# Kernel tuning notes

Hardware: AMD Instinct MI355X
Metric: run time of the kernel (lower is better)

The kernel has to match this reference:

```python
import jax, jax.numpy as jnp
import numpy as np

B, T = 128, 100
DZ, DA, DU, K, DOBS, H = 64, 32, 8, 8, 16, 128
JITTER = 1e-4  # _safe_cholesky: sym + jitter*I, then first try adds 1.0*jitter*I again


def setup_inputs() -> dict:
    key = jax.random.key(0)
    ks = jax.random.split(key, 10)
    eye_z = jnp.eye(DZ, dtype=jnp.float32)
    # stable-ish per-component transition matrices
    A_mats = 0.9 * eye_z[None] + 0.05 * jax.random.normal(ks[0], (K, DZ, DZ), jnp.float32)
    B_mats = 0.1 * jax.random.normal(ks[1], (K, DZ, DU), jnp.float32)
    C_mats = 0.3 * jax.random.normal(ks[2], (K, DA, DZ), jnp.float32)
    a_seq = jax.random.normal(ks[3], (B, T, DA), jnp.float32)
    h_obs = jax.random.normal(ks[4], (B, DOBS), jnp.float32)
    u_seq = jax.random.normal(ks[5], (B, T, DU), jnp.float32)
    mask = jnp.ones((B, T), jnp.float32)
    a_0 = jnp.zeros((1, DA), jnp.float32)          # nn.Parameter a_0
    P_0 = 10.0 * eye_z                              # 10 * eye(dim_z)
    Q = 0.05 * eye_z                                # Q_std * eye(dim_z)
    R = 0.05 * jnp.eye(DA, dtype=jnp.float32)       # R_std * eye(dim_a)
    din = DA + DOBS + DU
    s = 1.0 / float(np.sqrt(H))
    W_ih = s * jax.random.normal(ks[6], (3 * H, din), jnp.float32)
    W_hh = s * jax.random.normal(ks[7], (3 * H, H), jnp.float32)
    b_ih = jnp.zeros((3 * H,), jnp.float32)
    b_hh = jnp.zeros((3 * H,), jnp.float32)
    W_out = s * jax.random.normal(ks[8], (K, H), jnp.float32)
    b_out = jnp.zeros((K,), jnp.float32)
    return dict(a_seq=a_seq, h_obs=h_obs, u_seq=u_seq, mask=mask,
                A_mats=A_mats, B_mats=B_mats, C_mats=C_mats,
                a_0=a_0, P_0=P_0, Q=Q, R=R,
                W_ih=W_ih, W_hh=W_hh, b_ih=b_ih, b_hh=b_hh,
                W_out=W_out, b_out=b_out, epoch=100)


def _sym(M):
    return 0.5 * (M + jnp.swapaxes(M, -1, -2))


def _gru_alpha(x, h, W_ih, W_hh, b_ih, b_hh, W_out, b_out):
    # GRU-cell alpha_net: mixture weights over K components
    gi = x @ W_ih.T + b_ih
    gh = h @ W_hh.T + b_hh
    ir, iz, inn = jnp.split(gi, 3, axis=-1)
    hr, hz, hn = jnp.split(gh, 3, axis=-1)
    r = jax.nn.sigmoid(ir + hr)
    zg = jax.nn.sigmoid(iz + hz)
    n = jnp.tanh(inn + r * hn)
    h_new = (1.0 - zg) * n + zg * h
    alpha = jax.nn.softmax(h_new @ W_out.T + b_out, axis=-1)
    return alpha, h_new


def _kalman_forward(a_seq, h_obs, u_seq, mask, A_mats, B_mats, C_mats,
                    a_0, P_0, Q, R, W_ih, W_hh, b_ih, b_hh, W_out, b_out):
    Bsz = a_seq.shape[0]
    I = jnp.eye(DZ, dtype=a_seq.dtype)

    def mix(alpha):
        A = jnp.einsum('bk,kij->bij', alpha, A_mats)
        Bc = jnp.einsum('bk,kij->bij', alpha, B_mats)
        C = jnp.einsum('bk,kij->bij', alpha, C_mats)
        return A, Bc, C

    def alpha_net(a, u, h):
        x = jnp.concatenate([a, h_obs, u], axis=-1)
        return _gru_alpha(x, h, W_ih, W_hh, b_ih, b_hh, W_out, b_out)

    gru_h = jnp.zeros((Bsz, H), a_seq.dtype)
    a_prev = jnp.broadcast_to(a_0, (Bsz, DA))
    alpha0, gru_h = alpha_net(a_prev, u_seq[:, 0], gru_h)
    A_k0, B_k0, C_k0 = mix(alpha0)

    z0 = jnp.zeros((Bsz, DZ), a_seq.dtype)
    P0 = jnp.broadcast_to(P_0, (Bsz, DZ, DZ))

    def step(carry, inp):
        z_prev, P, h, A_k, B_k, C_k = carry
        a_k, u_k, m_k = inp  # [B,da], [B,du], [B]
        mk = m_k[:, None]
        # predict with matrices chosen at previous step
        z = jnp.einsum('bij,bj->bi', A_k, z_prev) + jnp.einsum('bij,bj->bi', B_k, u_k)
        a_hat = jnp.einsum('bij,bj->bi', C_k, z)
        r_k = a_k - a_hat
        CP = jnp.einsum('bij,bjk->bik', C_k, P)                      # C P
        S = jnp.einsum('bik,bjk->bij', CP, C_k) + R                   # C P C^T + R
        # K = solve(S^T, C P^T)^T  (i.e. K = P C^T S^{-1})
        CPt = jnp.einsum('bij,bkj->bik', C_k, P)
        Kg = jnp.swapaxes(jnp.linalg.solve(jnp.swapaxes(S, -1, -2), CPt), -1, -2)
        Kg = Kg * m_k[:, None, None]
        IKC = I - jnp.einsum('bij,bjk->bik', Kg, C_k)
        # Joseph form update
        P_filt = (jnp.einsum('bij,bjk,blk->bil', IKC, P, IKC)
                  + jnp.einsum('bij,jk,blk->bil', Kg, R, Kg))
        P_filt = _sym(P_filt)
        z_mean = z + jnp.einsum('bij,bj->bi', Kg, r_k)
        L = jnp.linalg.cholesky(_sym(P_filt) + 2.0 * JITTER * I)      # safe cholesky
        z_filt = z_mean                                               # dist.mean
        a_filt = jnp.einsum('bij,bj->bi', C_k, z_filt)
        a_k_hat = mk * a_k + (1.0 - mk) * a_filt
        C_old = C_k
        alpha, h = alpha_net(a_k_hat, u_k, h)
        A_n, B_n, C_n = mix(alpha)
        z_pred = (jnp.einsum('bij,bj->bi', A_n, z_filt)
                  + jnp.einsum('bij,bj->bi', B_n, u_k))
        a_pred = jnp.einsum('bij,bj->bi', C_n, z_pred)
        P_pred = _sym(jnp.einsum('bij,bjk,blk->bil', A_n, P_filt, A_n) + Q)
        carry = (z_filt, P_pred, h, A_n, B_n, C_n)
        out = (z_filt, P_filt, z_pred, P_pred, alpha, a_filt, a_pred,
               S, z_mean, L, A_n, B_n, C_old)
        return carry, out

    xs = (jnp.swapaxes(a_seq, 0, 1), jnp.swapaxes(u_seq, 0, 1), jnp.swapaxes(mask, 0, 1))
    _, outs = jax.lax.scan(step, (z0, P0, gru_h, A_k0, B_k0, C_k0), xs)
    # scan outputs are [T, B, ...] -> [B, T, ...]
    (z_filt, P_filt, z_pred, P_pred, alpha_seq, a_filt, a_pred,
     S_pred, z_means, z_scale_tril, A_seq, B_seq, C_seq) = jax.tree.map(
        lambda x: jnp.swapaxes(x, 0, 1), outs)
    return (z_filt, P_filt, z_pred, a_filt, a_pred, P_pred, alpha_seq,
            A_seq, B_seq, C_seq, z_means, z_scale_tril, S_pred)


def reference(a_seq, h_obs, u_seq, mask, A_mats, B_mats, C_mats,
              a_0, P_0, Q, R, W_ih, W_hh, b_ih, b_hh, W_out, b_out, epoch):
    # epoch >= warmup/burn-in thresholds (all 0), so no detach branches apply
    return _kalman_forward(a_seq, h_obs, u_seq, mask, A_mats, B_mats, C_mats,
                           a_0, P_0, Q, R, W_ih, W_hh, b_ih, b_hh, W_out, b_out)
```

## Files before the change

### kernel.cpp

```cpp
#include <hip/hip_runtime.h>

typedef float f4 __attribute__((ext_vector_type(4)));

#define NT 256
#define BB 128
#define BT 100
#define DZc 64
#define DAc 32
#define DUc 8
#define KMIX 8
#define DOBSc 16
#define HG 128
#define DINc 56

#define O_ZFILT   0LL
#define O_PFILT   819200LL
#define O_ZPRED   53248000LL
#define O_AFILT   54067200LL
#define O_APRED   54476800LL
#define O_PPRED   54886400LL
#define O_ALPHA   107315200LL
#define O_ASEQ    107417600LL
#define O_BSEQ    159846400LL
#define O_CSEQ    166400000LL
#define O_ZMEAN   192614400LL
#define O_LTRIL   193433600LL
#define O_SPRED   245862400LL

__device__ __forceinline__ float dot4(f4 a, f4 b) {
    return a[0]*b[0] + a[1]*b[1] + a[2]*b[2] + a[3]*b[3];
}

struct SMem {
    float P[DZc][68];
    float A[DZc][68];
    float AT[DZc][65];
    float Wk[DZc][68];
    float Qm[DZc][68];
    float C[DAc][68];
    float CP[DAc][68];
    float Xm[DAc][68];
    float S[DAc][33];
    float Rm[DAc][33];
    float dinv[DAc];
    float col[64];
    float Bm[DZc][8];
    float z[DZc], zp[DZc], zn[DZc];
    float h[HG], hn[HG];
    float gh[3*HG], gi[3*HG];
    float x[64];
    float ak[DAc], rvec[DAc];
    float akN[DAc];
    float ubuf[2][8];
    float mkN;
    float lg[8];
    float mk;
};

template<bool EMIT>
__device__ __forceinline__ void mix_apply(SMem& s, int tid, size_t bt, const float* al8,
    const float* __restrict__ A_mats, const float* __restrict__ B_mats,
    const float* __restrict__ C_mats, float* __restrict__ out)
{
    const f4* A4 = (const f4*)A_mats;
    const f4* B4 = (const f4*)B_mats;
    const f4* C4 = (const f4*)C_mats;
    #pragma unroll 2
    for (int e = 0; e < 4; ++e) {
        int i4 = tid + e*256;
        f4 acc = {0.f,0.f,0.f,0.f};
        #pragma unroll
        for (int k = 0; k < 8; ++k) acc += al8[k] * A4[k*1024 + i4];
        int row = i4 >> 4, cb = (i4 & 15) * 4;
        *(f4*)&s.A[row][cb] = acc;
        s.AT[cb][row] = acc[0]; s.AT[cb+1][row] = acc[1];
        s.AT[cb+2][row] = acc[2]; s.AT[cb+3][row] = acc[3];
        if (EMIT) *(f4*)&out[O_ASEQ + bt*4096 + (size_t)i4*4] = acc;
    }
    if (tid < 128) {
        int i4 = tid;
        f4 acc = {0.f,0.f,0.f,0.f};
        #pragma unroll
        for (int k = 0; k < 8; ++k) acc += al8[k] * B4[k*128 + i4];
        *(f4*)&s.Bm[i4>>1][(i4&1)*4] = acc;
        if (EMIT) *(f4*)&out[O_BSEQ + bt*512 + (size_t)i4*4] = acc;
    }
    #pragma unroll 1
    for (int e = 0; e < 2; ++e) {
        int i4 = tid + e*256;
        f4 acc = {0.f,0.f,0.f,0.f};
        #pragma unroll
        for (int k = 0; k < 8; ++k) acc += al8[k] * C4[k*512 + i4];
        *(f4*)&s.C[i4>>4][(i4&15)*4] = acc;
    }
}

__global__ void __launch_bounds__(NT, 1)
kalman_seq(const float* __restrict__ a_seq, const float* __restrict__ h_obs,
           const float* __restrict__ u_seq, const float* __restrict__ mask,
           const float* __restrict__ A_mats, const float* __restrict__ B_mats,
           const float* __restrict__ C_mats, const float* __restrict__ a_0,
           const float* __restrict__ P_0, const float* __restrict__ Q,
           const float* __restrict__ R, const float* __restrict__ W_ih,
           const float* __restrict__ W_hh, const float* __restrict__ b_ih,
           const float* __restrict__ b_hh, const float* __restrict__ W_out,
           const float* __restrict__ b_out, float* __restrict__ out)
{
    __shared__ SMem s;
    const int b = blockIdx.x;
    const int tid = threadIdx.x;
    const int r4 = (tid >> 4) << 2;
    const int c4 = (tid & 15) << 2;

    for (int idx = tid; idx < DZc*DZc; idx += NT) {
        s.P[idx >> 6][idx & 63]  = P_0[idx];
        s.Qm[idx >> 6][idx & 63] = Q[idx];
    }
    for (int idx = tid; idx < DAc*DAc; idx += NT) s.Rm[idx >> 5][idx & 31] = R[idx];
    if (tid < HG) s.h[tid] = 0.f;
    if (tid < DZc) { s.z[tid] = 0.f; s.zp[tid] = 0.f; }
    if (tid < DAc)                 s.x[tid] = a_0[tid];
    else if (tid < DAc + DOBSc)    s.x[tid] = h_obs[b*DOBSc + (tid - DAc)];
    else if (tid < DINc)           s.x[tid] = u_seq[(size_t)b*BT*DUc + (tid - DAc - DOBSc)];
    if (tid >= 128 && tid < 160)      s.akN[tid-128] = a_seq[(size_t)b*BT*DAc + (tid-128)];
    else if (tid >= 160 && tid < 168) { s.ubuf[0][tid-160] = u_seq[(size_t)b*BT*DUc + (tid-160)];
                                        s.ubuf[1][tid-160] = 0.f; }
    else if (tid == 168)              s.mkN = mask[(size_t)b*BT];
    __syncthreads();

    for (int g = tid; g < 3*HG; g += NT) {
        const float* wi = W_ih + (size_t)g * DINc;
        f4 ai = {0.f,0.f,0.f,0.f};
        #pragma unroll 7
        for (int q = 0; q < 14; ++q) ai += *(const f4*)(wi + q*4) * *(const f4*)&s.x[q*4];
        s.gi[g] = ai[0]+ai[1]+ai[2]+ai[3] + b_ih[g];
        s.gh[g] = b_hh[g];
    }
    __syncthreads();
    if (tid < HG) {
        float r  = 1.f / (1.f + expf(-(s.gi[tid] + s.gh[tid])));
        float zg = 1.f / (1.f + expf(-(s.gi[HG+tid] + s.gh[HG+tid])));
        float n  = tanhf(s.gi[2*HG+tid] + r * s.gh[2*HG+tid]);
        s.h[tid] = (1.f - zg) * n;
    }
    __syncthreads();
    if (tid < KMIX) {
        const float* wo = W_out + tid * HG;
        f4 acc = {0.f,0.f,0.f,0.f};
        #pragma unroll 8
        for (int q = 0; q < 32; ++q) acc += *(const f4*)(wo + q*4) * *(const f4*)&s.h[q*4];
        s.lg[tid] = acc[0]+acc[1]+acc[2]+acc[3] + b_out[tid];
    }
    __syncthreads();
    {
        float lg[8];
        #pragma unroll
        for (int k = 0; k < 8; ++k) lg[k] = s.lg[k];
        float mx = lg[0];
        #pragma unroll
        for (int k = 1; k < 8; ++k) mx = fmaxf(mx, lg[k]);
        float al[8]; float sum = 0.f;
        #pragma unroll
        for (int k = 0; k < 8; ++k) { al[k] = expf(lg[k] - mx); sum += al[k]; }
        float rs = 1.f / sum;
        #pragma unroll
        for (int k = 0; k < 8; ++k) al[k] *= rs;
        mix_apply<false>(s, tid, 0, al, A_mats, B_mats, C_mats, out);
    }
    __syncthreads();

    for (int t = 0; t < BT; ++t) {
        const size_t bt = (size_t)b * BT + t;
        const int cur = t & 1;

        if (tid < 64) {
            float acc = s.zp[tid];
            #pragma unroll
            for (int q = 0; q < DUc; ++q)
                acc += s.Bm[tid][q] * (s.ubuf[cur][q] - s.ubuf[cur^1][q]);
            s.zp[tid] = acc;
        } else if (tid < 96) {
            float av = s.akN[tid-64];
            s.ak[tid-64] = av;
            s.x[tid-64] = av;
        } else if (tid < 104) {
            s.x[48 + (tid-96)] = s.ubuf[cur][tid-96];
        } else if (tid == 104) {
            s.mk = s.mkN;
        }
        __syncthreads();
        const float mkv = s.mk;
        const bool mk1 = (mkv == 1.0f);

        {
            const int r = tid >> 3;
            const int c8 = (tid & 7) * 8;
            f4 acc0 = {0.f,0.f,0.f,0.f}, acc1 = {0.f,0.f,0.f,0.f};
            #pragma unroll 4
            for (int k4 = 0; k4 < 16; ++k4) {
                f4 cr = *(const f4*)&s.C[r][k4*4];
                #pragma unroll
                for (int kk = 0; kk < 4; ++kk) {
                    float cv = cr[kk];
                    acc0 += cv * *(const f4*)&s.P[k4*4+kk][c8];
                    acc1 += cv * *(const f4*)&s.P[k4*4+kk][c8+4];
                }
            }
            *(f4*)&s.CP[r][c8]   = acc0;
            *(f4*)&s.CP[r][c8+4] = acc1;
        }
        if (tid < DAc) {
            float acc = 0.f;
            #pragma unroll 4
            for (int k4 = 0; k4 < 16; ++k4)
                acc += dot4(*(const f4*)&s.C[tid][k4*4], *(const f4*)&s.zp[k4*4]);
            s.rvec[tid] = s.ak[tid] - acc;
        }
        __syncthreads();

        {
            const int r = tid >> 3;
            const int cb = (tid & 7) * 4;
            f4 acc = {0.f,0.f,0.f,0.f};
            #pragma unroll 4
            for (int k4 = 0; k4 < 16; ++k4) {
                f4 a = *(const f4*)&s.CP[r][k4*4];
                #pragma unroll
                for (int j = 0; j < 4; ++j)
                    acc[j] += dot4(a, *(const f4*)&s.C[cb+j][k4*4]);
            }
            f4 rm = {s.Rm[r][cb], s.Rm[r][cb+1], s.Rm[r][cb+2], s.Rm[r][cb+3]};
            f4 v = acc + rm;
            s.S[r][cb] = v[0]; s.S[r][cb+1] = v[1]; s.S[r][cb+2] = v[2]; s.S[r][cb+3] = v[3];
            *(f4*)&out[O_SPRED + bt*1024 + (size_t)r*32 + cb] = v;
        }
        __syncthreads();

        if (tid < 64) {
            const int lane = tid;
            const int l = lane & 31;
            float row[32];
            #pragma unroll
            for (int j = 0; j < 32; ++j) row[j] = s.S[l][j];
            #pragma unroll
            for (int k = 0; k < 32; ++k) {
                if (lane < 32) s.col[lane] = row[k];
                __threadfence_block();
                float cb[32];
                #pragma unroll
                for (int jv = 0; jv < 8; ++jv) {
                    if (jv*4 + 3 >= k) {
                        f4 cv = *(const f4*)&s.col[jv*4];
                        cb[jv*4] = cv[0]; cb[jv*4+1] = cv[1];
                        cb[jv*4+2] = cv[2]; cb[jv*4+3] = cv[3];
                    }
                }
                float dv = 1.0f / cb[k];
                if (lane == k) s.dinv[k] = dv;
                float fm = (l > k) ? (row[k] * dv) : 0.f;
                #pragma unroll
                for (int j = k+1; j < 32; ++j)
                    row[j] -= fm * cb[j];
                __threadfence_block();
            }
            if (lane < 32) {
                #pragma unroll
                for (int j = 0; j < 32; ++j) s.S[l][j] = row[j];
            }
            __threadfence_block();
            float v[32];
            #pragma unroll
            for (int r = 0; r < 32; ++r) v[r] = s.CP[r][lane];
            #pragma unroll
            for (int r = 0; r < 32; ++r) {
                float acc = v[r];
                #pragma unroll
                for (int k = 0; k < r; ++k) acc -= s.S[r][k] * v[k];
                v[r] = s.dinv[r] * acc;
            }
            #pragma unroll
            for (int r = 30; r >= 0; --r) {
                float acc = 0.f;
                #pragma unroll
                for (int k = r+1; k < 32; ++k) acc += s.S[k][r] * v[k];
                v[r] -= s.dinv[r] * acc;
            }
            float accz = 0.f;
            #pragma unroll
            for (int r = 0; r < 32; ++r) {
                s.Xm[r][lane] = v[r];
                accz += v[r] * s.rvec[r];
            }
            s.zn[lane] = s.zp[lane] + mkv * accz;
            __threadfence_block();
            if (lane < DAc) {
                float acc = 0.f;
                #pragma unroll 4
                for (int k4 = 0; k4 < 16; ++k4)
                    acc += dot4(*(const f4*)&s.C[lane][k4*4], *(const f4*)&s.zn[k4*4]);
                out[O_AFILT + bt*DAc + lane] = acc;
                if (!mk1) s.x[lane] = mkv * s.ak[lane] + (1.f - mkv) * acc;
            }
        } else if (tid < 192) {
            const int idx = tid - 64;
            const float* wir = W_ih + (size_t)idx * DINc;
            const float* wiz = W_ih + (size_t)(HG + idx) * DINc;
            const float* win = W_ih + (size_t)(2*HG + idx) * DINc;
            const float* whr = W_hh + (size_t)idx * HG;
            const float* whz = W_hh + (size_t)(HG + idx) * HG;
            const float* whn = W_hh + (size_t)(2*HG + idx) * HG;
            f4 air = {0.f,0.f,0.f,0.f}, aiz = {0.f,0.f,0.f,0.f}, ain = {0.f,0.f,0.f,0.f};
            #pragma unroll 4
            for (int q = 0; q < 14; ++q) {
                f4 xv = *(const f4*)&s.x[q*4];
                air += *(const f4*)(wir + q*4) * xv;
                aiz += *(const f4*)(wiz + q*4) * xv;
                ain += *(const f4*)(win + q*4) * xv;
            }
            f4 ahr = {0.f,0.f,0.f,0.f}, ahz = {0.f,0.f,0.f,0.f}, ahn = {0.f,0.f,0.f,0.f};
            #pragma unroll 4
            for (int q = 0; q < 32; ++q) {
                f4 hv = *(const f4*)&s.h[q*4];
                ahr += *(const f4*)(whr + q*4) * hv;
                ahz += *(const f4*)(whz + q*4) * hv;
                ahn += *(const f4*)(whn + q*4) * hv;
            }
            float gir = air[0]+air[1]+air[2]+air[3] + b_ih[idx];
            float giz = aiz[0]+aiz[1]+aiz[2]+aiz[3] + b_ih[HG + idx];
            float gin = ain[0]+ain[1]+ain[2]+ain[3] + b_ih[2*HG + idx];
            float ghr = ahr[0]+ahr[1]+ahr[2]+ahr[3] + b_hh[idx];
            float ghz = ahz[0]+ahz[1]+ahz[2]+ahz[3] + b_hh[HG + idx];
            float ghn = ahn[0]+ahn[1]+ahn[2]+ahn[3] + b_hh[2*HG + idx];
            float r  = 1.f / (1.f + expf(-(gir + ghr)));
            float zg = 1.f / (1.f + expf(-(giz + ghz)));
            float n  = tanhf(gin + r * ghn);
            s.hn[idx] = (1.f - zg) * n + zg * s.h[idx];
        } else {
            const int l = tid - 192;
            #pragma unroll 2
            for (int e = 0; e < 8; ++e) {
                int i4 = l + e*64;
                *(f4*)&out[O_CSEQ + bt*2048 + (size_t)i4*4] = *(const f4*)&s.C[i4>>4][(i4&15)*4];
            }
        }
        __syncthreads();

        float pfA = 0.f, pfU = 0.f, pfM = 0.f;
        {
            const int t2 = (t+1 < BT) ? (t+1) : t;
            const size_t bt2 = (size_t)b*BT + t2;
            if (tid >= 192 && tid < 224)      pfA = a_seq[bt2*DAc + (tid-192)];
            else if (tid >= 224 && tid < 232) pfU = u_seq[bt2*DUc + (tid-224)];
            else if (tid == 232)              pfM = mask[bt2];
        }

        {
            const float coef = (mkv*mkv - 2.f*mkv) * 0.5f;
            f4 acc0 = {0.f,0.f,0.f,0.f}, acc1 = {0.f,0.f,0.f,0.f};
            f4 acc2 = {0.f,0.f,0.f,0.f}, acc3 = {0.f,0.f,0.f,0.f};
            #pragma unroll 4
            for (int l = 0; l < DAc; ++l) {
                f4 cpc = *(const f4*)&s.CP[l][c4];
                f4 xc  = *(const f4*)&s.Xm[l][c4];
                f4 cpr = *(const f4*)&s.CP[l][r4];
                f4 xr  = *(const f4*)&s.Xm[l][r4];
                acc0 += xr[0]*cpc + cpr[0]*xc;
                acc1 += xr[1]*cpc + cpr[1]*xc;
                acc2 += xr[2]*cpc + cpr[2]*xc;
                acc3 += xr[3]*cpc + cpr[3]*xc;
            }
            #pragma unroll
            for (int i = 0; i < 4; ++i) {
                const int row = r4 + i;
                f4 g = (i==0) ? acc0 : (i==1) ? acc1 : (i==2) ? acc2 : acc3;
                f4 p = *(const f4*)&s.P[row][c4];
                f4 v = p + coef * g;
                *(f4*)&s.P[row][c4] = v;
                *(f4*)&out[O_PFILT + bt*4096 + (size_t)row*64 + c4] = v;
            }
        }
        if (tid < DZc) {
            float v = s.zn[tid];
            out[O_ZFILT + bt*DZc + tid] = v;
            out[O_ZMEAN + bt*DZc + tid] = v;
            s.z[tid] = v;
        }

        if (!mk1) {
            __syncthreads();
            for (int g = tid; g < 3*HG; g += NT) {
                const float* wi = W_ih + (size_t)g * DINc;
                const float* wh = W_hh + (size_t)g * HG;
                f4 ai = {0.f,0.f,0.f,0.f}, ah = {0.f,0.f,0.f,0.f};
                #pragma unroll 7
                for (int q = 0; q < 14; ++q) ai += *(const f4*)(wi + q*4) * *(const f4*)&s.x[q*4];
                #pragma unroll 8
                for (int q = 0; q < 32; ++q) ah += *(const f4*)(wh + q*4) * *(const f4*)&s.h[q*4];
                s.gi[g] = ai[0]+ai[1]+ai[2]+ai[3] + b_ih[g];
                s.gh[g] = ah[0]+ah[1]+ah[2]+ah[3] + b_hh[g];
            }
            __syncthreads();
            if (tid < HG) {
                float gi0 = s.gi[tid], gi1 = s.gi[HG+tid], gi2 = s.gi[2*HG+tid];
                float gh0 = s.gh[tid], gh1 = s.gh[HG+tid], gh2 = s.gh[2*HG+tid];
                float hold = s.h[tid];
                float r  = 1.f / (1.f + expf(-(gi0 + gh0)));
                float zg = 1.f / (1.f + expf(-(gi1 + gh1)));
                float n  = tanhf(gi2 + r * gh2);
                s.hn[tid] = (1.f - zg) * n + zg * hold;
            }
            __syncthreads();
        }

        {
            const int lane = tid & 63;
            const int g = lane >> 3;
            const int cb = (lane & 7) * 16;
            f4 a4 = {0.f,0.f,0.f,0.f};
            #pragma unroll
            for (int q = 0; q < 4; ++q)
                a4 += *(const f4*)(W_out + (size_t)g*HG + cb + q*4) * *(const f4*)&s.hn[cb + q*4];
            float acc = a4[0]+a4[1]+a4[2]+a4[3];
            acc += __shfl_xor(acc, 1); acc += __shfl_xor(acc, 2); acc += __shfl_xor(acc, 4);
            float lg[8];
            #pragma unroll
            for (int k = 0; k < 8; ++k) lg[k] = __shfl(acc, k*8) + b_out[k];
            float mx = lg[0];
            #pragma unroll
            for (int k = 1; k < 8; ++k) mx = fmaxf(mx, lg[k]);
            float al[8]; float sum = 0.f;
            #pragma unroll
            for (int k = 0; k < 8; ++k) { al[k] = expf(lg[k] - mx); sum += al[k]; }
            float rs = 1.f / sum;
            #pragma unroll
            for (int k = 0; k < 8; ++k) al[k] *= rs;
            if (tid < 8) out[O_ALPHA + bt*8 + tid] = al[tid];
            mix_apply<true>(s, tid, bt, al, A_mats, B_mats, C_mats, out);
        }
        if (tid < HG) s.h[tid] = s.hn[tid];
        __syncthreads();

        if (tid < 64) {
            float acc = 0.f;
            #pragma unroll 8
            for (int k = 0; k < DZc; ++k) acc += s.AT[k][tid] * s.z[k];
            #pragma unroll
            for (int q = 0; q < DUc; ++q) acc += s.Bm[tid][q] * s.ubuf[cur][q];
            s.zp[tid] = acc;
            out[O_ZPRED + bt*DZc + tid] = acc;
        }
        {
            f4 acc[4] = {{0.f,0.f,0.f,0.f},{0.f,0.f,0.f,0.f},{0.f,0.f,0.f,0.f},{0.f,0.f,0.f,0.f}};
            #pragma unroll 2
            for (int k4 = 0; k4 < 16; ++k4) {
                f4 ar0 = *(const f4*)&s.A[r4+0][k4*4];
                f4 ar1 = *(const f4*)&s.A[r4+1][k4*4];
                f4 ar2 = *(const f4*)&s.A[r4+2][k4*4];
                f4 ar3 = *(const f4*)&s.A[r4+3][k4*4];
                #pragma unroll
                for (int kk = 0; kk < 4; ++kk) {
                    f4 bv = *(const f4*)&s.P[k4*4+kk][c4];
                    acc[0] += ar0[kk] * bv; acc[1] += ar1[kk] * bv;
                    acc[2] += ar2[kk] * bv; acc[3] += ar3[kk] * bv;
                }
            }
            #pragma unroll
            for (int i = 0; i < 4; ++i)
                *(f4*)&s.Wk[r4+i][c4] = acc[i];
        }
        __syncthreads();

        {
            f4 acc[4] = {{0.f,0.f,0.f,0.f},{0.f,0.f,0.f,0.f},{0.f,0.f,0.f,0.f},{0.f,0.f,0.f,0.f}};
            #pragma unroll 2
            for (int k4 = 0; k4 < 16; ++k4) {
                f4 w0 = *(const f4*)&s.Wk[r4+0][k4*4];
                f4 w1 = *(const f4*)&s.Wk[r4+1][k4*4];
                f4 w2 = *(const f4*)&s.Wk[r4+2][k4*4];
                f4 w3 = *(const f4*)&s.Wk[r4+3][k4*4];
                #pragma unroll
                for (int kk = 0; kk < 4; ++kk) {
                    f4 av = *(const f4*)&s.AT[k4*4+kk][c4];
                    acc[0] += w0[kk] * av; acc[1] += w1[kk] * av;
                    acc[2] += w2[kk] * av; acc[3] += w3[kk] * av;
                }
            }
            #pragma unroll
            for (int i = 0; i < 4; ++i) {
                const int row = r4 + i;
                f4 q = *(const f4*)&s.Qm[row][c4];
                f4 v = acc[i] + q;
                *(f4*)&s.P[row][c4] = v;
                *(f4*)&out[O_PPRED + bt*4096 + (size_t)row*64 + c4] = v;
            }
        }
        if (tid < DAc) {
            float acc = 0.f;
            #pragma unroll 4
            for (int k4 = 0; k4 < 16; ++k4)
                acc += dot4(*(const f4*)&s.C[tid][k4*4], *(const f4*)&s.zp[k4*4]);
            out[O_APRED + bt*DAc + tid] = acc;
        }
        if (tid >= 192 && tid < 224)      s.akN[tid-192] = pfA;
        else if (tid >= 224 && tid < 232) s.ubuf[(t+1)&1][tid-224] = pfU;
        else if (tid == 232)              s.mkN = pfM;
        __syncthreads();
    }
}

__global__ void __launch_bounds__(64)
chol_batch(float* __restrict__ out)
{
    __shared__ float M[DZc][65];
    __shared__ float sd[DZc];
    const size_t bt = blockIdx.x;
    const int lane = threadIdx.x;
    const float* src = out + O_PFILT + bt*4096;
    #pragma unroll 4
    for (int e = 0; e < 16; ++e) {
        int i4 = lane + e*64;
        f4 v = *(const f4*)(src + (size_t)i4*4);
        int row = i4 >> 4, cb = (i4 & 15) * 4;
        M[row][cb] = v[0]; M[row][cb+1] = v[1]; M[row][cb+2] = v[2]; M[row][cb+3] = v[3];
    }
    __syncthreads();
    M[lane][lane] += 2.0e-4f;
    __syncthreads();
    for (int k = 0; k < DZc; ++k) {
        __threadfence_block();
        float mkk = M[k][k];
        if (lane == k) sd[k] = sqrtf(mkk);
        if (lane > k) {
            float f = M[lane][k] / mkk;
            for (int j = k + 1; j <= lane; ++j)
                M[lane][j] -= f * M[j][k];
        }
    }
    __threadfence_block();
    for (int k = 0; k < lane; ++k) M[lane][k] /= sd[k];
    M[lane][lane] = sd[lane];
    for (int k = lane + 1; k < DZc; ++k) M[lane][k] = 0.f;
    __syncthreads();
    float* dst = out + O_LTRIL + bt*4096;
    #pragma unroll 4
    for (int e = 0; e < 16; ++e) {
        int i4 = lane + e*64;
        int row = i4 >> 4, cb = (i4 & 15) * 4;
        f4 v = {M[row][cb], M[row][cb+1], M[row][cb+2], M[row][cb+3]};
        *(f4*)(dst + (size_t)i4*4) = v;
    }
}

extern "C" void kernel_launch(void* const* d_in, const int* in_sizes, int n_in,
                              void* d_out, int out_size, void* d_ws, size_t ws_size,
                              hipStream_t stream) {
    const float* a_seq  = (const float*)d_in[0];
    const float* h_obs  = (const float*)d_in[1];
    const float* u_seq  = (const float*)d_in[2];
    const float* mask   = (const float*)d_in[3];
    const float* A_mats = (const float*)d_in[4];
    const float* B_mats = (const float*)d_in[5];
    const float* C_mats = (const float*)d_in[6];
    const float* a_0    = (const float*)d_in[7];
    const float* P_0    = (const float*)d_in[8];
    const float* Q      = (const float*)d_in[9];
    const float* R      = (const float*)d_in[10];
    const float* W_ih   = (const float*)d_in[11];
    const float* W_hh   = (const float*)d_in[12];
    const float* b_ih   = (const float*)d_in[13];
    const float* b_hh   = (const float*)d_in[14];
    const float* W_out  = (const float*)d_in[15];
    const float* b_out  = (const float*)d_in[16];
    float* out = (float*)d_out;

    kalman_seq<<<dim3(BB), dim3(NT), 0, stream>>>(a_seq, h_obs, u_seq, mask,
        A_mats, B_mats, C_mats, a_0, P_0, Q, R, W_ih, W_hh, b_ih, b_hh, W_out, b_out, out);
    chol_batch<<<dim3(BB*BT), dim3(64), 0, stream>>>(out);
}
```

Measured before the change: 6.335 ms.

## Fold per-step input staging into previous step and double-buffer Cholesky column

New measurement: 6.328 ms. No clear change (-0.1%).

```diff
diff --git a/kernel.cpp b/kernel.cpp
--- a/kernel.cpp
+++ b/kernel.cpp
@@ -43,16 +43,14 @@
     float S[DAc][33];
     float Rm[DAc][33];
     float dinv[DAc];
-    float col[64];
+    float col[2][64];
     float Bm[DZc][8];
     float z[DZc], zp[DZc], zn[DZc];
     float h[HG], hn[HG];
     float gh[3*HG], gi[3*HG];
     float x[64];
     float ak[DAc], rvec[DAc];
-    float akN[DAc];
     float ubuf[2][8];
-    float mkN;
     float lg[8];
     float mk;
 };
@@ -118,14 +116,11 @@
     }
     for (int idx = tid; idx < DAc*DAc; idx += NT) s.Rm[idx >> 5][idx & 31] = R[idx];
     if (tid < HG) s.h[tid] = 0.f;
-    if (tid < DZc) { s.z[tid] = 0.f; s.zp[tid] = 0.f; }
+    if (tid < DZc) s.z[tid] = 0.f;
     if (tid < DAc)                 s.x[tid] = a_0[tid];
     else if (tid < DAc + DOBSc)    s.x[tid] = h_obs[b*DOBSc + (tid - DAc)];
     else if (tid < DINc)           s.x[tid] = u_seq[(size_t)b*BT*DUc + (tid - DAc - DOBSc)];
-    if (tid >= 128 && tid < 160)      s.akN[tid-128] = a_seq[(size_t)b*BT*DAc + (tid-128)];
-    else if (tid >= 160 && tid < 168) { s.ubuf[0][tid-160] = u_seq[(size_t)b*BT*DUc + (tid-160)];
-                                        s.ubuf[1][tid-160] = 0.f; }
-    else if (tid == 168)              s.mkN = mask[(size_t)b*BT];
+    if (tid >= 160 && tid < 168)   s.ubuf[0][tid-160] = u_seq[(size_t)b*BT*DUc + (tid-160)];
     __syncthreads();
 
     for (int g = tid; g < 3*HG; g += NT) {
@@ -169,26 +164,23 @@
     }
     __syncthreads();
 
+    if (tid < 64) {
+        float acc = 0.f;
+        #pragma unroll
+        for (int q = 0; q < DUc; ++q) acc += s.Bm[tid][q] * s.ubuf[0][q];
+        s.zp[tid] = acc;
+    } else if (tid < 96) {
+        float av = a_seq[(size_t)b*BT*DAc + (tid-64)];
+        s.ak[tid-64] = av;
+        s.x[tid-64] = av;
+    } else if (tid == 104) {
+        s.mk = mask[(size_t)b*BT];
+    }
+    __syncthreads();
+
     for (int t = 0; t < BT; ++t) {
         const size_t bt = (size_t)b * BT + t;
         const int cur = t & 1;
-
-        if (tid < 64) {
-            float acc = s.zp[tid];
-            #pragma unroll
-            for (int q = 0; q < DUc; ++q)
-                acc += s.Bm[tid][q] * (s.ubuf[cur][q] - s.ubuf[cur^1][q]);
-            s.zp[tid] = acc;
-        } else if (tid < 96) {
-            float av = s.akN[tid-64];
-            s.ak[tid-64] = av;
-            s.x[tid-64] = av;
-        } else if (tid < 104) {
-            s.x[48 + (tid-96)] = s.ubuf[cur][tid-96];
-        } else if (tid == 104) {
-            s.mk = s.mkN;
-        }
-        __syncthreads();
         const float mkv = s.mk;
         const bool mk1 = (mkv == 1.0f);
 
@@ -244,13 +236,13 @@
             for (int j = 0; j < 32; ++j) row[j] = s.S[l][j];
             #pragma unroll
             for (int k = 0; k < 32; ++k) {
-                if (lane < 32) s.col[lane] = row[k];
+                if (lane < 32) s.col[k & 1][lane] = row[k];
                 __threadfence_block();
                 float cb[32];
                 #pragma unroll
                 for (int jv = 0; jv < 8; ++jv) {
                     if (jv*4 + 3 >= k) {
-                        f4 cv = *(const f4*)&s.col[jv*4];
+                        f4 cv = *(const f4*)&s.col[k & 1][jv*4];
                         cb[jv*4] = cv[0]; cb[jv*4+1] = cv[1];
                         cb[jv*4+2] = cv[2]; cb[jv*4+3] = cv[3];
                     }
@@ -261,7 +253,6 @@
                 #pragma unroll
                 for (int j = k+1; j < 32; ++j)
                     row[j] -= fm * cb[j];
-                __threadfence_block();
             }
             if (lane < 32) {
                 #pragma unroll
@@ -385,6 +376,7 @@
             out[O_ZMEAN + bt*DZc + tid] = v;
             s.z[tid] = v;
         }
+        if (tid >= 224 && tid < 232) s.ubuf[(t+1)&1][tid-224] = pfU;
 
         if (!mk1) {
             __syncthreads();
@@ -446,8 +438,12 @@
             for (int k = 0; k < DZc; ++k) acc += s.AT[k][tid] * s.z[k];
             #pragma unroll
             for (int q = 0; q < DUc; ++q) acc += s.Bm[tid][q] * s.ubuf[cur][q];
+            out[O_ZPRED + bt*DZc + tid] = acc;
+            s.zn[tid] = acc;
+            #pragma unroll
+            for (int q = 0; q < DUc; ++q)
+                acc += s.Bm[tid][q] * (s.ubuf[cur^1][q] - s.ubuf[cur][q]);
             s.zp[tid] = acc;
-            out[O_ZPRED + bt*DZc + tid] = acc;
         }
         {
             f4 acc[4] = {{0.f,0.f,0.f,0.f},{0.f,0.f,0.f,0.f},{0.f,0.f,0.f,0.f},{0.f,0.f,0.f,0.f}};
@@ -498,12 +494,17 @@
             float acc = 0.f;
             #pragma unroll 4
             for (int k4 = 0; k4 < 16; ++k4)
-                acc += dot4(*(const f4*)&s.C[tid][k4*4], *(const f4*)&s.zp[k4*4]);
+                acc += dot4(*(const f4*)&s.C[tid][k4*4], *(const f4*)&s.zn[k4*4]);
             out[O_APRED + bt*DAc + tid] = acc;
         }
-        if (tid >= 192 && tid < 224)      s.akN[tid-192] = pfA;
-        else if (tid >= 224 && tid < 232) s.ubuf[(t+1)&1][tid-224] = pfU;
-        else if (tid == 232)              s.mkN = pfM;
+        if (tid >= 192 && tid < 224) {
+            s.ak[tid-192] = pfA;
+            s.x[tid-192]  = pfA;
+        } else if (tid >= 224 && tid < 232) {
+            s.x[48 + (tid-224)] = pfU;
+        } else if (tid == 232) {
+            s.mk = pfM;
+        }
         __syncthreads();
     }
 }
```
